# Kernel tuning notes

Measured on AMD Instinct MI355X. Metric: run time of the kernel, lower is better.

## Reference

```python
import jax, jax.numpy as jnp
import numpy as np

HIDDEN = 1024
HEADS = 16
GRAPH_N = 100


def setup_inputs() -> dict:
    key = jax.random.key(0)
    ks = jax.random.split(key, 16)
    B, S, D = 8, 512, HIDDEN
    inp = {
        "v": jax.random.normal(ks[0], (B, S, D), jnp.float32),
        "k": jax.random.normal(ks[1], (B, S, D), jnp.float32),
        "q": jax.random.normal(ks[2], (B, S, D), jnp.float32),
        "mask": jax.random.randint(ks[3], (B, 1, 1, S), 0, 2).astype(bool),
        "graph": jax.random.uniform(ks[4], (B, GRAPH_N, GRAPH_N), jnp.float32),
    }
    s = 1.0 / np.sqrt(D)
    inp["Wv"] = jax.random.normal(ks[5], (D, D), jnp.float32) * s
    inp["bv"] = jnp.zeros((D,), jnp.float32)
    inp["Wk"] = jax.random.normal(ks[6], (D, D), jnp.float32) * s
    inp["bk"] = jnp.zeros((D,), jnp.float32)
    inp["Wq"] = jax.random.normal(ks[7], (D, D), jnp.float32) * s
    inp["bq"] = jnp.zeros((D,), jnp.float32)
    inp["Wm"] = jax.random.normal(ks[8], (D, D), jnp.float32) * s
    inp["bm"] = jnp.zeros((D,), jnp.float32)
    return inp


def _split_heads(x, B, S):
    # (B, S, D) -> (B, H, S, dk)
    return x.reshape(B, S, HEADS, HIDDEN // HEADS).transpose(0, 2, 1, 3)


def reference(v, k, q, mask, graph, Wv, bv, Wk, bk, Wq, bq, Wm, bm):
    B, S, D = q.shape
    dk = D // HEADS

    vh = _split_heads(v @ Wv.T + bv, B, S)
    kh = _split_heads(k @ Wk.T + bk, B, S)
    qh = _split_heads(q @ Wq.T + bq, B, S)

    scores = jnp.einsum("bhqd,bhkd->bhqk", qh, kh) / jnp.sqrt(jnp.float32(dk))

    # graph + I, then (statically) pad to (B, S, S) with ones if S > 100
    g = graph + jnp.eye(GRAPH_N, dtype=graph.dtype)
    if S > GRAPH_N:
        g = jnp.ones((B, S, S), graph.dtype).at[:, :GRAPH_N, :GRAPH_N].set(g)

    causal_scores = scores * g[:, None, :, :]
    causal_scores = jnp.where(mask, jnp.float32(-1e9), causal_scores)
    att = jax.nn.softmax(causal_scores, axis=-1)  # dropout = identity (eval)

    out = jnp.einsum("bhqk,bhkd->bhqd", att, vh)
    out = out.transpose(0, 2, 1, 3).reshape(B, S, D)
    return out @ Wm.T + bm
```

## Files before the change

### kernel.cpp

```cpp
#include <hip/hip_runtime.h>
#include <hip/hip_bf16.h>
#include <math.h>

#define HIDDEN 1024
#define HEADS 16
#define DK 64
#define BB 8
#define SS 512
#define GN 100

typedef __attribute__((ext_vector_type(8))) short short8_t;
typedef __attribute__((ext_vector_type(4))) float f32x4;

__device__ __forceinline__ unsigned short f32_to_bf16_rne(float f) {
  unsigned int u = __float_as_uint(f);
  u += 0x7FFFu + ((u >> 16) & 1u);
  return (unsigned short)(u >> 16);
}
__device__ __forceinline__ float bf16_to_f32(unsigned short h) {
  return __uint_as_float(((unsigned int)h) << 16);
}

typedef const __attribute__((address_space(1))) void* gas_ptr;
typedef __attribute__((address_space(3))) void* las_ptr;
__device__ __forceinline__ void gl16(const void* g, void* l) {
  __builtin_amdgcn_global_load_lds((gas_ptr)g, (las_ptr)l, 16, 0, 0);
}

__global__ __launch_bounds__(256) void round_all(
    const float* __restrict__ s0, const float* __restrict__ s1,
    const float* __restrict__ s2, const float* __restrict__ s3,
    const float* __restrict__ s4, const float* __restrict__ s5,
    const float* __restrict__ s6,
    unsigned short* __restrict__ d0, unsigned short* __restrict__ d1,
    unsigned short* __restrict__ d2, unsigned short* __restrict__ d3,
    unsigned short* __restrict__ d4, unsigned short* __restrict__ d5,
    unsigned short* __restrict__ d6,
    const unsigned int* __restrict__ mask_raw, unsigned char* __restrict__ mask_dec,
    int nBig, int nW) {
  const int z = blockIdx.y;
  if (z == 7) {
    if (blockIdx.x != 0) return;
    __shared__ int s_isBytes;
    if (threadIdx.x == 0) s_isBytes = 0;
    __syncthreads();
    const int n = BB * SS;
    int local = 0;
    for (int i = threadIdx.x; i < n / 4; i += 256)
      if (mask_raw[i] > 1u) local = 1;
    if (local) atomicOr(&s_isBytes, 1);
    __syncthreads();
    const int isBytes = s_isBytes;
    for (int i = threadIdx.x; i < n; i += 256) {
      unsigned char v;
      if (isBytes)
        v = (unsigned char)((mask_raw[i >> 2] >> ((i & 3) * 8)) & 0xFFu);
      else
        v = (unsigned char)(mask_raw[i] & 1u);
      mask_dec[i] = v;
    }
    return;
  }
  const float* src = z == 0 ? s0 : z == 1 ? s1 : z == 2 ? s2 : z == 3 ? s3
                   : z == 4 ? s4 : z == 5 ? s5 : s6;
  unsigned short* dst = z == 0 ? d0 : z == 1 ? d1 : z == 2 ? d2 : z == 3 ? d3
                      : z == 4 ? d4 : z == 5 ? d5 : d6;
  const int n8 = z < 3 ? nBig : nW;
  const int idx = blockIdx.x * 256 + threadIdx.x;
  if (idx >= n8) return;
  const float4* s = (const float4*)src + (size_t)idx * 2;
  const float4 x0 = s[0], x1 = s[1];
  const float xs[8] = {x0.x, x0.y, x0.z, x0.w, x1.x, x1.y, x1.z, x1.w};
  unsigned int p[4];
  #pragma unroll
  for (int i = 0; i < 4; ++i)
    p[i] = (unsigned int)f32_to_bf16_rne(xs[2 * i]) |
           ((unsigned int)f32_to_bf16_rne(xs[2 * i + 1]) << 16);
  uint4 v = {p[0], p[1], p[2], p[3]};
  *((uint4*)dst + idx) = v;
}


__global__ __launch_bounds__(256) void gemm_qkv(
    const unsigned short* __restrict__ A0, const unsigned short* __restrict__ A1,
    const unsigned short* __restrict__ A2,
    const unsigned short* __restrict__ B0, const unsigned short* __restrict__ B1,
    const unsigned short* __restrict__ B2,
    const float* __restrict__ bias0, const float* __restrict__ bias1,
    const float* __restrict__ bias2,
    unsigned short* __restrict__ C0, unsigned short* __restrict__ C1,
    unsigned short* __restrict__ C2) {
  __shared__ __align__(16) unsigned short As[128][64];
  __shared__ __align__(16) unsigned short Bs[128][64];

  const int wgid = blockIdx.x;
  const int xcd = wgid & 7, i0 = wgid >> 3;
  const int z = i0 >> 5;
  const int r0 = i0 & 31;
  const int by = xcd * 4 + (r0 >> 3);
  const int bx = r0 & 7;

  const unsigned short* __restrict__ A = z == 0 ? A0 : z == 1 ? A1 : A2;
  const unsigned short* __restrict__ B = z == 0 ? B0 : z == 1 ? B1 : B2;
  const float* __restrict__ bias = z == 0 ? bias0 : z == 1 ? bias1 : bias2;
  unsigned short* __restrict__ C = z == 0 ? C0 : z == 1 ? C1 : C2;

  const int tid = threadIdx.x;
  const int brow0 = by * 128, bcol0 = bx * 128;
  const int w = tid >> 6, l = tid & 63;
  const int wr = w >> 1, wc = w & 1;
  const int l15 = l & 15, l4 = l >> 4;

  f32x4 acc[4][4];
  const f32x4 fzero = {0.f, 0.f, 0.f, 0.f};
  #pragma unroll
  for (int i = 0; i < 4; ++i)
    #pragma unroll
    for (int j = 0; j < 4; ++j) acc[i][j] = fzero;

  const unsigned short* gA = A + (size_t)(brow0 + w * 32 + (l >> 3)) * HIDDEN + (l & 7) * 8;
  const unsigned short* gB = B + (size_t)(bcol0 + w * 32 + (l >> 3)) * HIDDEN + (l & 7) * 8;

  for (int kt = 0; kt < 16; ++kt) {
    const int ko = kt * 64;
    #pragma unroll
    for (int j = 0; j < 4; ++j) {
      gl16(gA + (size_t)j * 8 * HIDDEN + ko, &As[w * 32 + j * 8][0]);
      gl16(gB + (size_t)j * 8 * HIDDEN + ko, &Bs[w * 32 + j * 8][0]);
    }
    __syncthreads();

    #pragma unroll
    for (int s = 0; s < 2; ++s) {
      short8_t af[4], bf[4];
      const int co = s * 32 + l4 * 8;
      #pragma unroll
      for (int i = 0; i < 4; ++i) {
        af[i] = *(const short8_t*)&As[wr * 64 + i * 16 + l15][co];
        bf[i] = *(const short8_t*)&Bs[wc * 64 + i * 16 + l15][co];
      }
      #pragma unroll
      for (int i = 0; i < 4; ++i)
        #pragma unroll
        for (int j = 0; j < 4; ++j)
          acc[i][j] = __builtin_amdgcn_mfma_f32_16x16x32_bf16(af[i], bf[j], acc[i][j], 0, 0, 0);
    }
    __syncthreads();
  }

  unsigned short* cs = &As[0][0];
  #pragma unroll
  for (int i = 0; i < 4; ++i)
    #pragma unroll
    for (int j = 0; j < 4; ++j) {
      const int colL = wc * 64 + j * 16 + l15;
      const float bc = bias[bcol0 + colL];
      #pragma unroll
      for (int r = 0; r < 4; ++r) {
        const int rowL = wr * 64 + i * 16 + l4 * 4 + r;
        cs[rowL * 128 + colL] = f32_to_bf16_rne(acc[i][j][r] + bc);
      }
    }
  __syncthreads();
  #pragma unroll
  for (int t2 = 0; t2 < 8; ++t2) {
    const int rowL = t2 * 16 + (tid >> 4);
    const int colL = (tid & 15) * 8;
    const uint4 val = *(const uint4*)&cs[rowL * 128 + colL];
    *(uint4*)(C + (size_t)(brow0 + rowL) * HIDDEN + bcol0 + colL) = val;
  }
}

__global__ __launch_bounds__(256) void gemm_out(
    const unsigned short* __restrict__ A, const unsigned short* __restrict__ B,
    const float* __restrict__ bias, float* __restrict__ C) {
  __shared__ __align__(16) unsigned short As[128][64];
  __shared__ __align__(16) unsigned short Bs[128][64];

  const int wgid = blockIdx.x;
  const int xcd = wgid & 7, i0 = wgid >> 3;
  const int by = xcd * 4 + (i0 >> 3);
  const int bx = i0 & 7;

  const int tid = threadIdx.x;
  const int brow0 = by * 128, bcol0 = bx * 128;
  const int w = tid >> 6, l = tid & 63;
  const int wr = w >> 1, wc = w & 1;
  const int l15 = l & 15, l4 = l >> 4;

  f32x4 acc[4][4];
  const f32x4 fzero = {0.f, 0.f, 0.f, 0.f};
  #pragma unroll
  for (int i = 0; i < 4; ++i)
    #pragma unroll
    for (int j = 0; j < 4; ++j) acc[i][j] = fzero;

  const unsigned short* gA = A + (size_t)(brow0 + w * 32 + (l >> 3)) * HIDDEN + (l & 7) * 8;
  const unsigned short* gB = B + (size_t)(bcol0 + w * 32 + (l >> 3)) * HIDDEN + (l & 7) * 8;

  for (int kt = 0; kt < 16; ++kt) {
    const int ko = kt * 64;
    #pragma unroll
    for (int j = 0; j < 4; ++j) {
      gl16(gA + (size_t)j * 8 * HIDDEN + ko, &As[w * 32 + j * 8][0]);
      gl16(gB + (size_t)j * 8 * HIDDEN + ko, &Bs[w * 32 + j * 8][0]);
    }
    __syncthreads();

    #pragma unroll
    for (int s = 0; s < 2; ++s) {
      short8_t af[4], bf[4];
      const int co = s * 32 + l4 * 8;
      #pragma unroll
      for (int i = 0; i < 4; ++i) {
        af[i] = *(const short8_t*)&As[wr * 64 + i * 16 + l15][co];
        bf[i] = *(const short8_t*)&Bs[wc * 64 + i * 16 + l15][co];
      }
      #pragma unroll
      for (int i = 0; i < 4; ++i)
        #pragma unroll
        for (int j = 0; j < 4; ++j)
          acc[i][j] = __builtin_amdgcn_mfma_f32_16x16x32_bf16(af[i], bf[j], acc[i][j], 0, 0, 0);
    }
    __syncthreads();
  }

  #pragma unroll
  for (int i = 0; i < 4; ++i)
    #pragma unroll
    for (int j = 0; j < 4; ++j) {
      const int col = bcol0 + wc * 64 + j * 16 + l15;
      const float bc = bias[col];
      #pragma unroll
      for (int r = 0; r < 4; ++r) {
        const int row = brow0 + wr * 64 + i * 16 + l4 * 4 + r;
        C[(size_t)row * HIDDEN + col] = acc[i][j][r] + bc;
      }
    }
}

__global__ __launch_bounds__(256) void vtrans(
    const unsigned short* __restrict__ Vphi, unsigned short* __restrict__ Vthi) {
  __shared__ __align__(16) unsigned short th[64][72];
  const int bh = blockIdx.x;
  const int b = bh >> 4, h = bh & 15;
  const int tid = threadIdx.x;
  const int lr = tid >> 2, lc = tid & 3;
  const int dr = tid >> 2, sq = tid & 3;

  for (int st = 0; st < 8; ++st) {
    const int s0 = st * 64;
    const size_t gi = ((size_t)(b * SS + s0 + lr)) * HIDDEN + h * DK + lc * 16;
    const uint4* ph = (const uint4*)(Vphi + gi);
    *(uint4*)&th[lr][lc * 16] = ph[0];
    *(uint4*)&th[lr][lc * 16 + 8] = ph[1];
    __syncthreads();

    unsigned short oh[16];
    #pragma unroll
    for (int ss = 0; ss < 16; ++ss) oh[ss] = th[sq * 16 + ss][dr];
    const size_t go = ((size_t)(bh * DK + dr)) * SS + s0 + sq * 16;
    *(uint4*)(Vthi + go) = *(uint4*)&oh[0];
    *(uint4*)(Vthi + go + 8) = *(uint4*)&oh[8];
    __syncthreads();
  }
}

__global__ __launch_bounds__(256) void flash_attn(
    const unsigned short* __restrict__ Qp, const unsigned short* __restrict__ Kp,
    const unsigned short* __restrict__ Vt, const unsigned char* __restrict__ mask,
    const float* __restrict__ graph, unsigned short* __restrict__ Ohi) {
  __shared__ __align__(16) unsigned short Ks[2][64][64];
  __shared__ __align__(16) unsigned short Vs[2][64][64];
  __shared__ __align__(16) unsigned short Plds[4096];

  const int qt = blockIdx.x, bh = blockIdx.y;
  const int b = bh >> 4, h = bh & 15;
  const int tid = threadIdx.x;
  const int w = tid >> 6, l = tid & 63;
  const int l15 = l & 15, l4 = l >> 4;
  const int qw = w * 16;
  const int q0 = qt * 64;

  short8_t qf[2];
  #pragma unroll
  for (int ks = 0; ks < 2; ++ks)
    qf[ks] = *(const short8_t*)(Qp +
        ((size_t)(b * SS + q0 + qw + l15)) * HIDDEN + h * DK + ks * 32 + l4 * 8);

  f32x4 acc[4];
  const f32x4 fzero = {0.f, 0.f, 0.f, 0.f};
  #pragma unroll
  for (int n = 0; n < 4; ++n) acc[n] = fzero;
  float rs[4] = {};

  const int srow = tid >> 2;
  const int sslot = (tid & 3) * 2;
  const unsigned short* kg0 = Kp + ((size_t)(b * SS + srow)) * HIDDEN + h * DK + sslot * 8;
  const unsigned short* vg0 = Vt + ((size_t)(bh * DK + srow)) * SS + sslot * 8;
  const int sw0 = (sslot ^ (srow & 7)) * 8;
  const int sw1 = ((sslot + 1) ^ (srow & 7)) * 8;

  uint4 kr0 = *(const uint4*)kg0, kr1 = *(const uint4*)(kg0 + 8);
  uint4 vr0 = *(const uint4*)vg0, vr1 = *(const uint4*)(vg0 + 8);

  int p = 0;
  for (int kt = 0; kt < 8; ++kt, p ^= 1) {
    *(uint4*)&Ks[p][srow][sw0] = kr0;
    *(uint4*)&Ks[p][srow][sw1] = kr1;
    *(uint4*)&Vs[p][srow][sw0] = vr0;
    *(uint4*)&Vs[p][srow][sw1] = vr1;
    __syncthreads();

    if (kt < 7) {
      const unsigned short* kg = kg0 + (size_t)(kt + 1) * 64 * HIDDEN;
      const unsigned short* vg = vg0 + (kt + 1) * 64;
      kr0 = *(const uint4*)kg; kr1 = *(const uint4*)(kg + 8);
      vr0 = *(const uint4*)vg; vr1 = *(const uint4*)(vg + 8);
    }

    f32x4 sc[4];
    __builtin_amdgcn_s_setprio(1);
    #pragma unroll
    for (int n = 0; n < 4; ++n) {
      f32x4 s = fzero;
      #pragma unroll
      for (int ks = 0; ks < 2; ++ks) {
        const short8_t kf = *(const short8_t*)
            &Ks[p][n * 16 + l15][((ks * 4 + l4) ^ (l15 & 7)) * 8];
        s = __builtin_amdgcn_mfma_f32_16x16x32_bf16(qf[ks], kf, s, 0, 0, 0);
      }
      sc[n] = s;
    }
    __builtin_amdgcn_s_setprio(0);

    #pragma unroll
    for (int n = 0; n < 4; ++n) {
      const int ki = kt * 64 + n * 16 + l15;
      const bool mj = mask[b * SS + ki] != 0;
      const int kg_ = (n & 1) * 2 + (l15 >> 3);
      #pragma unroll
      for (int r = 0; r < 4; ++r) {
        float val = sc[n][r] * 0.125f;
        if (q0 < GN && kt < 2) {
          const int qi = q0 + qw + l4 * 4 + r;
          if (qi < GN && ki < GN)
            val *= graph[((size_t)b * GN + qi) * GN + ki] + (qi == ki ? 1.0f : 0.0f);
        }
        const float pv = mj ? 0.0f : __expf(val - 16.0f);
        rs[r] += pv;
        const int q = qw + l4 * 4 + r;
        const int idx = (n >> 1) * 2048 + ((q * 4 + (kg_ ^ ((q >> 2) & 3))) << 3) + (l15 & 7);
        Plds[idx] = f32_to_bf16_rne(pv);
      }
    }
    __syncthreads();

    __builtin_amdgcn_s_setprio(1);
    {
      const int q = qw + l15;
      #pragma unroll
      for (int ks = 0; ks < 2; ++ks) {
        const short8_t pa = *(const short8_t*)
            &Plds[ks * 2048 + ((q * 4 + (l4 ^ ((q >> 2) & 3))) << 3)];
        #pragma unroll
        for (int n2 = 0; n2 < 4; ++n2) {
          const short8_t vb = *(const short8_t*)
              &Vs[p][n2 * 16 + l15][((ks * 4 + l4) ^ (l15 & 7)) * 8];
          acc[n2] = __builtin_amdgcn_mfma_f32_16x16x32_bf16(pa, vb, acc[n2], 0, 0, 0);
        }
      }
    }
    __builtin_amdgcn_s_setprio(0);
  }

  float inv[4];
  #pragma unroll
  for (int r = 0; r < 4; ++r) {
    float vsum = rs[r];
    vsum += __shfl_xor(vsum, 1);
    vsum += __shfl_xor(vsum, 2);
    vsum += __shfl_xor(vsum, 4);
    vsum += __shfl_xor(vsum, 8);
    inv[r] = 1.0f / vsum;
  }

  #pragma unroll
  for (int n2 = 0; n2 < 4; ++n2) {
    const int col = h * DK + n2 * 16 + l15;
    #pragma unroll
    for (int r = 0; r < 4; ++r) {
      const int row = q0 + qw + l4 * 4 + r;
      const float val = acc[n2][r] * inv[r];
      Ohi[((size_t)(b * SS + row)) * HIDDEN + col] = f32_to_bf16_rne(val);
    }
  }
}

extern "C" void kernel_launch(void* const* d_in, const int* in_sizes, int n_in,
                              void* d_out, int out_size, void* d_ws, size_t ws_size,
                              hipStream_t stream) {
  const float* v     = (const float*)d_in[0];
  const float* k     = (const float*)d_in[1];
  const float* q     = (const float*)d_in[2];
  const unsigned int* mask_raw = (const unsigned int*)d_in[3];
  const float* graph = (const float*)d_in[4];
  const float* Wv = (const float*)d_in[5];
  const float* bv = (const float*)d_in[6];
  const float* Wk = (const float*)d_in[7];
  const float* bk = (const float*)d_in[8];
  const float* Wq = (const float*)d_in[9];
  const float* bq = (const float*)d_in[10];
  const float* Wm = (const float*)d_in[11];
  const float* bm = (const float*)d_in[12];
  float* out = (float*)d_out;

  const size_t MT = (size_t)BB * SS * HIDDEN;
  const size_t WT = (size_t)HIDDEN * HIDDEN;

  char* ws = (char*)d_ws;
  unsigned short* v_bf  = (unsigned short*)ws;  ws += MT * 2;
  unsigned short* k_bf  = (unsigned short*)ws;  ws += MT * 2;
  unsigned short* q_bf  = (unsigned short*)ws;  ws += MT * 2;
  unsigned short* Wv_bf = (unsigned short*)ws;  ws += WT * 2;
  unsigned short* Wk_bf = (unsigned short*)ws;  ws += WT * 2;
  unsigned short* Wq_bf = (unsigned short*)ws;  ws += WT * 2;
  unsigned short* Wm_bf = (unsigned short*)ws;  ws += WT * 2;
  unsigned short* Vp    = (unsigned short*)ws;  ws += MT * 2;
  unsigned short* Kp    = (unsigned short*)ws;  ws += MT * 2;
  unsigned short* Qp    = (unsigned short*)ws;  ws += MT * 2;
  unsigned short* Vt    = (unsigned short*)ws;  ws += MT * 2;
  unsigned char* mask_dec = (unsigned char*)ws; ws += 4096;
  unsigned short* at_bf = v_bf;

  const int nIn8 = (int)(MT / 8);
  const int nW8  = (int)(WT / 8);

  round_all<<<dim3(2048, 8), 256, 0, stream>>>(
      v, k, q, Wv, Wk, Wq, Wm,
      v_bf, k_bf, q_bf, Wv_bf, Wk_bf, Wq_bf, Wm_bf,
      mask_raw, mask_dec, nIn8, nW8);

  gemm_qkv<<<dim3(768), 256, 0, stream>>>(
      v_bf, k_bf, q_bf, Wv_bf, Wk_bf, Wq_bf, bv, bk, bq, Vp, Kp, Qp);

  vtrans<<<dim3(BB * HEADS), 256, 0, stream>>>(Vp, Vt);

  flash_attn<<<dim3(SS / 64, BB * HEADS), 256, 0, stream>>>(
      Qp, Kp, Vt, mask_dec, graph, at_bf);

  gemm_out<<<dim3(256), 256, 0, stream>>>(at_bf, Wm_bf, bm, out);
}
```

Measured before the change: 231.2 us.

## Fuse V transpose into QKV GEMM epilogue and halve GEMM tile width

The QKV and output GEMMs now use 128x64 tiles instead of 128x128, doubling the grid (1536 and 512 workgroups) so more CUs are busy. For the V projection, the epilogue writes the tile transposed through padded LDS straight into the per-head Vt layout, so the separate vtrans kernel and the Vp buffer go away. In exchange each tile gets less reuse of its loaded data, and the transposed stores are 64-byte row segments.

```diff
diff --git a/kernel.cpp b/kernel.cpp
--- a/kernel.cpp
+++ b/kernel.cpp
@@ -88,138 +88,163 @@
     const unsigned short* __restrict__ B2,
     const float* __restrict__ bias0, const float* __restrict__ bias1,
     const float* __restrict__ bias2,
-    unsigned short* __restrict__ C0, unsigned short* __restrict__ C1,
+    unsigned short* __restrict__ Vt, unsigned short* __restrict__ C1,
     unsigned short* __restrict__ C2) {
-  __shared__ __align__(16) unsigned short As[128][64];
-  __shared__ __align__(16) unsigned short Bs[128][64];
+  __shared__ __align__(16) unsigned short smem[12288];
 
   const int wgid = blockIdx.x;
   const int xcd = wgid & 7, i0 = wgid >> 3;
-  const int z = i0 >> 5;
-  const int r0 = i0 & 31;
-  const int by = xcd * 4 + (r0 >> 3);
-  const int bx = r0 & 7;
+  const int z = i0 >> 6;
+  const int r0 = i0 & 63;
+  const int by = xcd * 4 + (r0 >> 4);
+  const int bx = r0 & 15;
 
   const unsigned short* __restrict__ A = z == 0 ? A0 : z == 1 ? A1 : A2;
   const unsigned short* __restrict__ B = z == 0 ? B0 : z == 1 ? B1 : B2;
   const float* __restrict__ bias = z == 0 ? bias0 : z == 1 ? bias1 : bias2;
-  unsigned short* __restrict__ C = z == 0 ? C0 : z == 1 ? C1 : C2;
 
   const int tid = threadIdx.x;
-  const int brow0 = by * 128, bcol0 = bx * 128;
+  const int brow0 = by * 128, bcol0 = bx * 64;
   const int w = tid >> 6, l = tid & 63;
   const int wr = w >> 1, wc = w & 1;
   const int l15 = l & 15, l4 = l >> 4;
-
-  f32x4 acc[4][4];
+  const int lr = l >> 3, lc = (l & 7) * 8;
+
+  f32x4 acc[4][2];
   const f32x4 fzero = {0.f, 0.f, 0.f, 0.f};
   #pragma unroll
   for (int i = 0; i < 4; ++i)
     #pragma unroll
-    for (int j = 0; j < 4; ++j) acc[i][j] = fzero;
-
-  const unsigned short* gA = A + (size_t)(brow0 + w * 32 + (l >> 3)) * HIDDEN + (l & 7) * 8;
-  const unsigned short* gB = B + (size_t)(bcol0 + w * 32 + (l >> 3)) * HIDDEN + (l & 7) * 8;
+    for (int j = 0; j < 2; ++j) acc[i][j] = fzero;
+
+  const unsigned short* gA = A + (size_t)(brow0 + w * 32 + lr) * HIDDEN + lc;
+  const unsigned short* gB = B + (size_t)(bcol0 + w * 16 + lr) * HIDDEN + lc;
 
   for (int kt = 0; kt < 16; ++kt) {
     const int ko = kt * 64;
     #pragma unroll
-    for (int j = 0; j < 4; ++j) {
-      gl16(gA + (size_t)j * 8 * HIDDEN + ko, &As[w * 32 + j * 8][0]);
-      gl16(gB + (size_t)j * 8 * HIDDEN + ko, &Bs[w * 32 + j * 8][0]);
-    }
+    for (int j = 0; j < 4; ++j)
+      gl16(gA + (size_t)j * 8 * HIDDEN + ko, &smem[(w * 32 + j * 8) * 64]);
+    #pragma unroll
+    for (int j = 0; j < 2; ++j)
+      gl16(gB + (size_t)j * 8 * HIDDEN + ko, &smem[8192 + (w * 16 + j * 8) * 64]);
     __syncthreads();
 
     #pragma unroll
     for (int s = 0; s < 2; ++s) {
-      short8_t af[4], bf[4];
+      short8_t af[4], bf[2];
       const int co = s * 32 + l4 * 8;
       #pragma unroll
-      for (int i = 0; i < 4; ++i) {
-        af[i] = *(const short8_t*)&As[wr * 64 + i * 16 + l15][co];
-        bf[i] = *(const short8_t*)&Bs[wc * 64 + i * 16 + l15][co];
-      }
+      for (int i = 0; i < 4; ++i)
+        af[i] = *(const short8_t*)&smem[(wr * 64 + i * 16 + l15) * 64 + co];
+      #pragma unroll
+      for (int j = 0; j < 2; ++j)
+        bf[j] = *(const short8_t*)&smem[8192 + (wc * 32 + j * 16 + l15) * 64 + co];
       #pragma unroll
       for (int i = 0; i < 4; ++i)
         #pragma unroll
-        for (int j = 0; j < 4; ++j)
+        for (int j = 0; j < 2; ++j)
           acc[i][j] = __builtin_amdgcn_mfma_f32_16x16x32_bf16(af[i], bf[j], acc[i][j], 0, 0, 0);
     }
     __syncthreads();
   }
 
-  unsigned short* cs = &As[0][0];
-  #pragma unroll
-  for (int i = 0; i < 4; ++i)
-    #pragma unroll
-    for (int j = 0; j < 4; ++j) {
-      const int colL = wc * 64 + j * 16 + l15;
-      const float bc = bias[bcol0 + colL];
-      #pragma unroll
-      for (int r = 0; r < 4; ++r) {
-        const int rowL = wr * 64 + i * 16 + l4 * 4 + r;
-        cs[rowL * 128 + colL] = f32_to_bf16_rne(acc[i][j][r] + bc);
-      }
-    }
-  __syncthreads();
-  #pragma unroll
-  for (int t2 = 0; t2 < 8; ++t2) {
-    const int rowL = t2 * 16 + (tid >> 4);
-    const int colL = (tid & 15) * 8;
-    const uint4 val = *(const uint4*)&cs[rowL * 128 + colL];
-    *(uint4*)(C + (size_t)(brow0 + rowL) * HIDDEN + bcol0 + colL) = val;
+  if (z == 0) {
+    #pragma unroll
+    for (int i = 0; i < 4; ++i)
+      #pragma unroll
+      for (int j = 0; j < 2; ++j) {
+        const int colL = wc * 32 + j * 16 + l15;
+        const float bc = bias[bcol0 + colL];
+        #pragma unroll
+        for (int r = 0; r < 4; ++r) {
+          const int rowL = wr * 64 + i * 16 + l4 * 4 + r;
+          smem[colL * 136 + rowL] = f32_to_bf16_rne(acc[i][j][r] + bc);
+        }
+      }
+    __syncthreads();
+    const int d = tid >> 2, sq = tid & 3;
+    const int b = brow0 >> 9, sl0 = brow0 & 511;
+    const size_t go = ((size_t)(b * 16 + bx) * 64 + d) * SS + sl0 + sq * 32;
+    #pragma unroll
+    for (int q4 = 0; q4 < 4; ++q4)
+      *(uint4*)(Vt + go + q4 * 8) = *(const uint4*)&smem[d * 136 + sq * 32 + q4 * 8];
+  } else {
+    unsigned short* __restrict__ C = z == 1 ? C1 : C2;
+    #pragma unroll
+    for (int i = 0; i < 4; ++i)
+      #pragma unroll
+      for (int j = 0; j < 2; ++j) {
+        const int colL = wc * 32 + j * 16 + l15;
+        const float bc = bias[bcol0 + colL];
+        #pragma unroll
+        for (int r = 0; r < 4; ++r) {
+          const int rowL = wr * 64 + i * 16 + l4 * 4 + r;
+          smem[rowL * 64 + colL] = f32_to_bf16_rne(acc[i][j][r] + bc);
+        }
+      }
+    __syncthreads();
+    #pragma unroll
+    for (int t2 = 0; t2 < 4; ++t2) {
+      const int idx = t2 * 256 + tid;
+      const int row = idx >> 3, col = (idx & 7) * 8;
+      const uint4 val = *(const uint4*)&smem[row * 64 + col];
+      *(uint4*)(C + (size_t)(brow0 + row) * HIDDEN + bcol0 + col) = val;
+    }
   }
 }
 
 __global__ __launch_bounds__(256) void gemm_out(
     const unsigned short* __restrict__ A, const unsigned short* __restrict__ B,
     const float* __restrict__ bias, float* __restrict__ C) {
-  __shared__ __align__(16) unsigned short As[128][64];
-  __shared__ __align__(16) unsigned short Bs[128][64];
+  __shared__ __align__(16) unsigned short smem[12288];
 
   const int wgid = blockIdx.x;
   const int xcd = wgid & 7, i0 = wgid >> 3;
-  const int by = xcd * 4 + (i0 >> 3);
-  const int bx = i0 & 7;
+  const int by = xcd * 4 + (i0 >> 4);
+  const int bx = i0 & 15;
 
   const int tid = threadIdx.x;
-  const int brow0 = by * 128, bcol0 = bx * 128;
+  const int brow0 = by * 128, bcol0 = bx * 64;
   const int w = tid >> 6, l = tid & 63;
   const int wr = w >> 1, wc = w & 1;
   const int l15 = l & 15, l4 = l >> 4;
-
-  f32x4 acc[4][4];
+  const int lr = l >> 3, lc = (l & 7) * 8;
+
+  f32x4 acc[4][2];
   const f32x4 fzero = {0.f, 0.f, 0.f, 0.f};
   #pragma unroll
   for (int i = 0; i < 4; ++i)
     #pragma unroll
-    for (int j = 0; j < 4; ++j) acc[i][j] = fzero;
-
-  const unsigned short* gA = A + (size_t)(brow0 + w * 32 + (l >> 3)) * HIDDEN + (l & 7) * 8;
-  const unsigned short* gB = B + (size_t)(bcol0 + w * 32 + (l >> 3)) * HIDDEN + (l & 7) * 8;
+    for (int j = 0; j < 2; ++j) acc[i][j] = fzero;
+
+  const unsigned short* gA = A + (size_t)(brow0 + w * 32 + lr) * HIDDEN + lc;
+  const unsigned short* gB = B + (size_t)(bcol0 + w * 16 + lr) * HIDDEN + lc;
 
   for (int kt = 0; kt < 16; ++kt) {
     const int ko = kt * 64;
     #pragma unroll
-    for (int j = 0; j < 4; ++j) {
-      gl16(gA + (size_t)j * 8 * HIDDEN + ko, &As[w * 32 + j * 8][0]);
-      gl16(gB + (size_t)j * 8 * HIDDEN + ko, &Bs[w * 32 + j * 8][0]);
-    }
+    for (int j = 0; j < 4; ++j)
+      gl16(gA + (size_t)j * 8 * HIDDEN + ko, &smem[(w * 32 + j * 8) * 64]);
+    #pragma unroll
+    for (int j = 0; j < 2; ++j)
+      gl16(gB + (size_t)j * 8 * HIDDEN + ko, &smem[8192 + (w * 16 + j * 8) * 64]);
     __syncthreads();
 
     #pragma unroll
     for (int s = 0; s < 2; ++s) {
-      short8_t af[4], bf[4];
+      short8_t af[4], bf[2];
       const int co = s * 32 + l4 * 8;
       #pragma unroll
-      for (int i = 0; i < 4; ++i) {
-        af[i] = *(const short8_t*)&As[wr * 64 + i * 16 + l15][co];
-        bf[i] = *(const short8_t*)&Bs[wc * 64 + i * 16 + l15][co];
-      }
+      for (int i = 0; i < 4; ++i)
+        af[i] = *(const short8_t*)&smem[(wr * 64 + i * 16 + l15) * 64 + co];
+      #pragma unroll
+      for (int j = 0; j < 2; ++j)
+        bf[j] = *(const short8_t*)&smem[8192 + (wc * 32 + j * 16 + l15) * 64 + co];
       #pragma unroll
       for (int i = 0; i < 4; ++i)
         #pragma unroll
-        for (int j = 0; j < 4; ++j)
+        for (int j = 0; j < 2; ++j)
           acc[i][j] = __builtin_amdgcn_mfma_f32_16x16x32_bf16(af[i], bf[j], acc[i][j], 0, 0, 0);
     }
     __syncthreads();
@@ -228,8 +253,8 @@
   #pragma unroll
   for (int i = 0; i < 4; ++i)
     #pragma unroll
-    for (int j = 0; j < 4; ++j) {
-      const int col = bcol0 + wc * 64 + j * 16 + l15;
+    for (int j = 0; j < 2; ++j) {
+      const int col = bcol0 + wc * 32 + j * 16 + l15;
       const float bc = bias[col];
       #pragma unroll
       for (int r = 0; r < 4; ++r) {
@@ -237,33 +262,6 @@
         C[(size_t)row * HIDDEN + col] = acc[i][j][r] + bc;
       }
     }
-}
-
-__global__ __launch_bounds__(256) void vtrans(
-    const unsigned short* __restrict__ Vphi, unsigned short* __restrict__ Vthi) {
-  __shared__ __align__(16) unsigned short th[64][72];
-  const int bh = blockIdx.x;
-  const int b = bh >> 4, h = bh & 15;
-  const int tid = threadIdx.x;
-  const int lr = tid >> 2, lc = tid & 3;
-  const int dr = tid >> 2, sq = tid & 3;
-
-  for (int st = 0; st < 8; ++st) {
-    const int s0 = st * 64;
-    const size_t gi = ((size_t)(b * SS + s0 + lr)) * HIDDEN + h * DK + lc * 16;
-    const uint4* ph = (const uint4*)(Vphi + gi);
-    *(uint4*)&th[lr][lc * 16] = ph[0];
-    *(uint4*)&th[lr][lc * 16 + 8] = ph[1];
-    __syncthreads();
-
-    unsigned short oh[16];
-    #pragma unroll
-    for (int ss = 0; ss < 16; ++ss) oh[ss] = th[sq * 16 + ss][dr];
-    const size_t go = ((size_t)(bh * DK + dr)) * SS + s0 + sq * 16;
-    *(uint4*)(Vthi + go) = *(uint4*)&oh[0];
-    *(uint4*)(Vthi + go + 8) = *(uint4*)&oh[8];
-    __syncthreads();
-  }
 }
 
 __global__ __launch_bounds__(256) void flash_attn(
@@ -426,7 +424,6 @@
   unsigned short* Wk_bf = (unsigned short*)ws;  ws += WT * 2;
   unsigned short* Wq_bf = (unsigned short*)ws;  ws += WT * 2;
   unsigned short* Wm_bf = (unsigned short*)ws;  ws += WT * 2;
-  unsigned short* Vp    = (unsigned short*)ws;  ws += MT * 2;
   unsigned short* Kp    = (unsigned short*)ws;  ws += MT * 2;
   unsigned short* Qp    = (unsigned short*)ws;  ws += MT * 2;
   unsigned short* Vt    = (unsigned short*)ws;  ws += MT * 2;
@@ -441,13 +438,11 @@
       v_bf, k_bf, q_bf, Wv_bf, Wk_bf, Wq_bf, Wm_bf,
       mask_raw, mask_dec, nIn8, nW8);
 
-  gemm_qkv<<<dim3(768), 256, 0, stream>>>(
-      v_bf, k_bf, q_bf, Wv_bf, Wk_bf, Wq_bf, bv, bk, bq, Vp, Kp, Qp);
-
-  vtrans<<<dim3(BB * HEADS), 256, 0, stream>>>(Vp, Vt);
+  gemm_qkv<<<dim3(1536), 256, 0, stream>>>(
+      v_bf, k_bf, q_bf, Wv_bf, Wk_bf, Wq_bf, bv, bk, bq, Vt, Kp, Qp);
 
   flash_attn<<<dim3(SS / 64, BB * HEADS), 256, 0, stream>>>(
       Qp, Kp, Vt, mask_dec, graph, at_bf);
 
-  gemm_out<<<dim3(256), 256, 0, stream>>>(at_bf, Wm_bf, bm, out);
-}
+  gemm_out<<<dim3(512), 256, 0, stream>>>(at_bf, Wm_bf, bm, out);
+}
```

After: 230.3 us. No clear change (-0.4%).
